# Kernel optimization log

Measured on AMD Instinct MI355X. Metric: run time of the kernel, lower is better.

Reference implementation:

```python
import jax, jax.numpy as jnp
import numpy as np

TAU = 20.0
TH = 1.5
TAU_ADAPT = 100.0
BETA_ADAPT = 1.5
V_RESET = -0.5
SURR_SLOPE = 10.0


def setup_inputs() -> dict:
    key = jax.random.key(0)
    B, L, K = 32, 1024, 512
    I = jax.random.normal(key, (B, L, K), dtype=jnp.float32)
    return {"I": I}


def reference(I):
    # I: [B, L, K]
    B, L, K = I.shape
    dtype = I.dtype

    def step(carry, I_t):
        v, a, s_num = carry  # each [B, K]
        th_eff = TH + BETA_ADAPT * a
        v = v + (-v / TAU + I_t)            # membrane before reset
        s_soft = jax.nn.sigmoid(SURR_SLOPE * (v - th_eff))
        s_hard = (v >= th_eff).astype(dtype)
        # straight-through estimator: value = s_hard, grad flows via s_soft
        s = jax.lax.stop_gradient(s_hard - s_soft) + s_soft
        s_num = s_num + s
        s_det = jax.lax.stop_gradient(s)    # reset uses detached spike
        v_next = v * (1.0 - s_det) + V_RESET * s_det
        a_next = a + (-a / TAU_ADAPT + s)
        return (v_next, a_next, s_num), (s, s_num, v)

    zeros = jnp.zeros((B, K), dtype=dtype)
    init = (zeros, zeros, zeros)
    I_t_first = jnp.swapaxes(I, 0, 1)  # [L, B, K]
    _, (spikes, series, v_seq) = jax.lax.scan(step, init, I_t_first)
    # back to [B, L, K]
    spikes = jnp.swapaxes(spikes, 0, 1)
    series = jnp.swapaxes(series, 0, 1)
    v_seq = jnp.swapaxes(v_seq, 0, 1)
    return (spikes, series, v_seq)
```

## Files before the change

kernel.cpp:

```cpp
#include <hip/hip_runtime.h>


namespace {
constexpr int kL = 1024;
constexpr int kK = 512;
constexpr size_t kN = (size_t)32 * kL * kK;
constexpr float kVD = 1.0f - 1.0f / 20.0f;
constexpr float kAD = 1.0f - 1.0f / 100.0f;
}

template <int W, bool STORE, bool PFETCH>
__device__ __forceinline__ void slab16(const float* __restrict__ ip,
                                       unsigned& ioff,
                                       float* __restrict__ outp, unsigned& off,
                                       float (&ibuf)[16], float& v, float& a,
                                       float& snum, float& th) {
#pragma unroll
    for (int j = 0; j < 16; ++j) {
        const float It = ibuf[j];
        if (PFETCH) { ibuf[j] = ip[ioff]; ioff += kK; }
        v = __fmaf_rn(v, kVD, It);
        const bool fire = (v >= th);
        const float s = fire ? 1.0f : 0.0f;
        snum += s;
        if (STORE) {
            const float val = (W == 0) ? s : (W == 1) ? snum : v;
            __builtin_nontemporal_store(val, outp + off);
        }
        v = fire ? -0.5f : v;
        a = __fmaf_rn(a, kAD, s);
        th = __fmaf_rn(1.5f, a, 1.5f);
        off += kK;
    }
}

template <int W, int PAR>
__device__ __forceinline__ void run_chain(const float* __restrict__ ip,
                                          float* __restrict__ outp) {
    float v = 0.0f, a = 0.0f, snum = 0.0f, th = 1.5f;

    float ibufA[16], ibufB[16];
#pragma unroll
    for (int j = 0; j < 16; ++j) ibufA[j] = ip[(size_t)j * kK];
#pragma unroll
    for (int j = 0; j < 16; ++j) ibufB[j] = ip[(size_t)(16 + j) * kK];
    unsigned ioff = 32u * kK;
    unsigned off = 0;

#pragma unroll 1
    for (int c = 0; c < 31; ++c) {
        slab16<W, PAR == 0, true>(ip, ioff, outp, off, ibufA, v, a, snum, th);
        slab16<W, PAR == 1, true>(ip, ioff, outp, off, ibufB, v, a, snum, th);
    }
    slab16<W, PAR == 0, false>(ip, ioff, outp, off, ibufA, v, a, snum, th);
    slab16<W, PAR == 1, false>(ip, ioff, outp, off, ibufB, v, a, snum, th);
}

__global__ __launch_bounds__(384) void multilif_fwd(const float* __restrict__ I,
                                                    float* __restrict__ out) {
    const int lane = (int)threadIdx.x & 63;
    const int w = (int)threadIdx.x >> 6;
    const int wb0 = (int)blockIdx.x * 64;
    const size_t base = (size_t)(wb0 >> 9) * ((size_t)kL * kK)
                      + (size_t)(wb0 & (kK - 1)) + (size_t)lane;
    const float* __restrict__ ip = I + base;
    float* __restrict__ outp = out + (size_t)(w >> 1) * kN + base;

    switch (w) {
        case 0: run_chain<0, 0>(ip, outp); break;
        case 1: run_chain<0, 1>(ip, outp); break;
        case 2: run_chain<1, 0>(ip, outp); break;
        case 3: run_chain<1, 1>(ip, outp); break;
        case 4: run_chain<2, 0>(ip, outp); break;
        default: run_chain<2, 1>(ip, outp); break;
    }
}

extern "C" void kernel_launch(void* const* d_in, const int* in_sizes, int n_in,
                              void* d_out, int out_size, void* d_ws, size_t ws_size,
                              hipStream_t stream) {
    const float* I = (const float*)d_in[0];
    float* out = (float*)d_out;
    dim3 grid((32 * kK) / 64), block(384);
    hipLaunchKernelGGL(multilif_fwd, grid, block, 0, stream, I, out);
}
```

Measured before the change: 50.85 us.

## Add dedicated loader wave feeding LDS ring buffer to six consumer waves

Adds a seventh wave per block that loads input slabs with vectorised float4 global loads into an 8-slot LDS ring, synchronised with s_barrier each slab. The six scan waves then read inputs from LDS instead of each issuing its own redundant scalar global loads. This removes the six-fold duplicated global reads and moves latency hiding into a producer/consumer pipeline. In exchange it adds a block-wide barrier per 16-step slab, LDS traffic, and occupancy pressure from the 32KB ring and the larger block.

```diff
diff --git a/kernel.cpp b/kernel.cpp
--- a/kernel.cpp
+++ b/kernel.cpp
@@ -7,18 +7,73 @@
 constexpr size_t kN = (size_t)32 * kL * kK;
 constexpr float kVD = 1.0f - 1.0f / 20.0f;
 constexpr float kAD = 1.0f - 1.0f / 100.0f;
+constexpr int kSlabSteps = 16;
+constexpr int kRing = 8;
+constexpr int kSlabFloats = kSlabSteps * 64;
 }
 
-template <int W, bool STORE, bool PFETCH>
-__device__ __forceinline__ void slab16(const float* __restrict__ ip,
-                                       unsigned& ioff,
-                                       float* __restrict__ outp, unsigned& off,
-                                       float (&ibuf)[16], float& v, float& a,
-                                       float& snum, float& th) {
+__device__ __forceinline__ void issue_slab(const float* __restrict__ gq,
+                                           float4 (&r)[4]) {
+#pragma unroll
+    for (int q = 0; q < 4; ++q)
+        r[q] = *reinterpret_cast<const float4*>(gq + (size_t)q * 4 * kK);
+}
+
+__device__ __forceinline__ void write_slab(float* __restrict__ ring, int slot,
+                                           int lane, const float4 (&r)[4]) {
+    float* b = ring + (slot << 10) + (lane << 2);
+#pragma unroll
+    for (int q = 0; q < 4; ++q)
+        *reinterpret_cast<float4*>(b + (q << 8)) = r[q];
+}
+
+__device__ __forceinline__ void run_loader(const float* __restrict__ gp,
+                                           float* __restrict__ ring,
+                                           const int lane) {
+    float4 rr[kRing][4];
+#pragma unroll
+    for (int k = 0; k < 8; ++k)
+        issue_slab(gp + (size_t)k * kSlabSteps * kK, rr[k]);
+    write_slab(ring, 0, lane, rr[0]);
+    asm volatile("s_waitcnt lgkmcnt(0)" ::: "memory");
+#pragma unroll 1
+    for (int c = 0; c < 7; ++c) {
+#pragma unroll
+        for (int k = 0; k < 8; ++k) {
+            const int s = c * 8 + k;
+            __builtin_amdgcn_s_barrier();
+            asm volatile("" ::: "memory");
+            issue_slab(gp + (size_t)(s + 8) * kSlabSteps * kK, rr[k]);
+            write_slab(ring, (k + 1) & 7, lane, rr[(k + 1) & 7]);
+            asm volatile("s_waitcnt lgkmcnt(0)" ::: "memory");
+        }
+    }
+#pragma unroll
+    for (int k = 0; k < 8; ++k) {
+        __builtin_amdgcn_s_barrier();
+        asm volatile("" ::: "memory");
+        if (k < 7) {
+            write_slab(ring, (k + 1) & 7, lane, rr[(k + 1) & 7]);
+            asm volatile("s_waitcnt lgkmcnt(0)" ::: "memory");
+        }
+    }
+}
+
+template <int W, bool STORE>
+__device__ __forceinline__ void eat_slab(const float* __restrict__ ring,
+                                         const int slot, const int lane,
+                                         float* __restrict__ outp,
+                                         unsigned& off, float& v, float& a,
+                                         float& snum, float& th) {
+    __builtin_amdgcn_s_barrier();
+    asm volatile("" ::: "memory");
+    const float* rb = ring + (slot << 10) + lane;
+    float ib[16];
+#pragma unroll
+    for (int j = 0; j < 16; ++j) ib[j] = rb[j << 6];
 #pragma unroll
     for (int j = 0; j < 16; ++j) {
-        const float It = ibuf[j];
-        if (PFETCH) { ibuf[j] = ip[ioff]; ioff += kK; }
+        const float It = ib[j];
         v = __fmaf_rn(v, kVD, It);
         const bool fire = (v >= th);
         const float s = fire ? 1.0f : 0.0f;
@@ -35,44 +90,42 @@
 }
 
 template <int W, int PAR>
-__device__ __forceinline__ void run_chain(const float* __restrict__ ip,
-                                          float* __restrict__ outp) {
+__device__ __forceinline__ void run_consumer(const float* __restrict__ ring,
+                                             const int lane,
+                                             float* __restrict__ outp) {
     float v = 0.0f, a = 0.0f, snum = 0.0f, th = 1.5f;
-
-    float ibufA[16], ibufB[16];
-#pragma unroll
-    for (int j = 0; j < 16; ++j) ibufA[j] = ip[(size_t)j * kK];
-#pragma unroll
-    for (int j = 0; j < 16; ++j) ibufB[j] = ip[(size_t)(16 + j) * kK];
-    unsigned ioff = 32u * kK;
     unsigned off = 0;
-
 #pragma unroll 1
-    for (int c = 0; c < 31; ++c) {
-        slab16<W, PAR == 0, true>(ip, ioff, outp, off, ibufA, v, a, snum, th);
-        slab16<W, PAR == 1, true>(ip, ioff, outp, off, ibufB, v, a, snum, th);
+    for (int p = 0; p < 32; ++p) {
+        eat_slab<W, PAR == 0>(ring, (2 * p) & 7, lane, outp, off, v, a, snum, th);
+        eat_slab<W, PAR == 1>(ring, (2 * p + 1) & 7, lane, outp, off, v, a, snum, th);
     }
-    slab16<W, PAR == 0, false>(ip, ioff, outp, off, ibufA, v, a, snum, th);
-    slab16<W, PAR == 1, false>(ip, ioff, outp, off, ibufB, v, a, snum, th);
 }
 
-__global__ __launch_bounds__(384) void multilif_fwd(const float* __restrict__ I,
-                                                    float* __restrict__ out) {
+__global__ __launch_bounds__(448, 2) void multilif_fwd(
+        const float* __restrict__ I, float* __restrict__ out) {
+    __shared__ __align__(16) float ring[kRing * kSlabFloats];
     const int lane = (int)threadIdx.x & 63;
     const int w = (int)threadIdx.x >> 6;
     const int wb0 = (int)blockIdx.x * 64;
-    const size_t base = (size_t)(wb0 >> 9) * ((size_t)kL * kK)
-                      + (size_t)(wb0 & (kK - 1)) + (size_t)lane;
-    const float* __restrict__ ip = I + base;
-    float* __restrict__ outp = out + (size_t)(w >> 1) * kN + base;
+    const size_t cb = (size_t)(wb0 >> 9) * ((size_t)kL * kK)
+                    + (size_t)(wb0 & (kK - 1));
 
-    switch (w) {
-        case 0: run_chain<0, 0>(ip, outp); break;
-        case 1: run_chain<0, 1>(ip, outp); break;
-        case 2: run_chain<1, 0>(ip, outp); break;
-        case 3: run_chain<1, 1>(ip, outp); break;
-        case 4: run_chain<2, 0>(ip, outp); break;
-        default: run_chain<2, 1>(ip, outp); break;
+    if (w == 0) {
+        const float* gp = I + cb + (size_t)(lane >> 4) * kK
+                        + (size_t)((lane & 15) << 2);
+        run_loader(gp, ring, lane);
+        return;
+    }
+    const int cw = w - 1;
+    float* outp = out + (size_t)(cw >> 1) * kN + cb + (size_t)lane;
+    switch (cw) {
+        case 0: run_consumer<0, 0>(ring, lane, outp); break;
+        case 1: run_consumer<0, 1>(ring, lane, outp); break;
+        case 2: run_consumer<1, 0>(ring, lane, outp); break;
+        case 3: run_consumer<1, 1>(ring, lane, outp); break;
+        case 4: run_consumer<2, 0>(ring, lane, outp); break;
+        default: run_consumer<2, 1>(ring, lane, outp); break;
     }
 }
 
@@ -81,6 +134,6 @@
                               hipStream_t stream) {
     const float* I = (const float*)d_in[0];
     float* out = (float*)d_out;
-    dim3 grid((32 * kK) / 64), block(384);
+    dim3 grid((32 * kK) / 64), block(448);
     hipLaunchKernelGGL(multilif_fwd, grid, block, 0, stream, I, out);
 }
```

Result: slower. 58.41 us (+14.9%).
